# Optimization experiments

Measured on AMD Instinct MI355X. Metric: run time of the kernel, lower is better.

## Reference

```python
import jax, jax.numpy as jnp
import numpy as np


def setup_inputs() -> dict:
    key = jax.random.key(0)
    ks = jax.random.split(key, 5)
    B, T, C = 4, 2048, 2048
    n_heads = 16
    sc = 0.02
    return {
        "x": jax.random.normal(ks[0], (B, T, C), dtype=jnp.float32),
        "Wqkv": jax.random.normal(ks[1], (3 * C, C), dtype=jnp.float32) * sc,
        "bqkv": jax.random.normal(ks[2], (3 * C,), dtype=jnp.float32) * sc,
        "Wout": jax.random.normal(ks[3], (C, C), dtype=jnp.float32) * sc,
        "bout": jax.random.normal(ks[4], (C,), dtype=jnp.float32) * sc,
        "n_heads": n_heads,
    }


def reference(x, Wqkv, bqkv, Wout, bout, n_heads):
    B, T, C = x.shape
    hd = C // n_heads
    qkv = x @ Wqkv.T + bqkv                      # [B, T, 3C]
    q, k, v = jnp.split(qkv, 3, axis=-1)
    # [B, T, C] -> [B, nH, T, hd]
    def heads(t):
        return t.reshape(B, T, n_heads, hd).transpose(0, 2, 1, 3)
    q, k, v = heads(q), heads(k), heads(v)
    new_k, new_v = k, v
    att = jnp.einsum('bhqd,bhkd->bhqk', q, k) / jnp.sqrt(jnp.float32(hd))
    T_total = k.shape[2]
    # torch.tril(ones(T, T_total)): allow j <= i (standard causal when T_total == T)
    mask = jnp.tril(jnp.ones((T, T_total), dtype=bool))
    att = jnp.where(mask, att, -jnp.inf)
    att = jax.nn.softmax(att, axis=-1)
    y = jnp.einsum('bhqk,bhkd->bhqd', att, v)    # [B, nH, T, hd]
    y = y.transpose(0, 2, 1, 3).reshape(B, T, C)
    y = y @ Wout.T + bout
    return (y, new_k, new_v)
```

## Files before the change

kernel.cpp:

```cpp
#include <hip/hip_runtime.h>
#include <hip/hip_bf16.h>

typedef __attribute__((ext_vector_type(8))) short bf16x8;
typedef __attribute__((ext_vector_type(4))) float f32x4;

__device__ __forceinline__ unsigned short f2bf(float f) {
  unsigned u = __float_as_uint(f);
  u += 0x7fffu + ((u >> 16) & 1u);
  return (unsigned short)(u >> 16);
}

__device__ __forceinline__ void gload16(const void* g, void* l) {
  __builtin_amdgcn_global_load_lds(
      (const __attribute__((address_space(1))) void*)g,
      (__attribute__((address_space(3))) void*)l, 16, 0, 0);
}

__global__ void cvt_bf16(const float* __restrict__ in, unsigned short* __restrict__ out, int n4) {
  int i = blockIdx.x * blockDim.x + threadIdx.x;
  int st = gridDim.x * blockDim.x;
  for (; i < n4; i += st) {
    float4 f = ((const float4*)in)[i];
    ushort4 o;
    o.x = f2bf(f.x); o.y = f2bf(f.y); o.z = f2bf(f.z); o.w = f2bf(f.w);
    ((ushort4*)out)[i] = o;
  }
}

template<int EPI>
__global__ __launch_bounds__(512, 2) void gemm_bt(
    const unsigned short* __restrict__ A,
    const unsigned short* __restrict__ B,
    const float* __restrict__ bias,
    float* __restrict__ outF,
    unsigned short* __restrict__ q_ws,
    unsigned short* __restrict__ k_ws,
    unsigned short* __restrict__ v_wst,
    float* __restrict__ out_k,
    float* __restrict__ out_v,
    int M, int N, int K)
{
  __shared__ __align__(16) unsigned short As[2][16384];
  __shared__ __align__(16) unsigned short Bs[2][16384];

  const int nbx = N >> 8;
  int nwg = gridDim.x;
  int bid = blockIdx.x;
  int cpx = nwg >> 3;
  int sw  = (bid & 7) * cpx + (bid >> 3);
  int bx = sw % nbx, by = sw / nbx;
  const int m0 = by << 8, n0 = bx << 8;

  const int tid = threadIdx.x, w = tid >> 6, ln = tid & 63;
  const int wm = w >> 2, wn = w & 3;
  const int lg = ln >> 4, lc = ln & 15;

  const int srow = tid >> 3;
  const int scol = ((ln & 7) ^ (srow & 7)) * 8;

  f32x4 acc[8][4] = {};

  auto STAGE = [&](int bf, int k0) {
#pragma unroll
    for (int i = 0; i < 4; ++i)
      gload16(A + (size_t)(m0 + i * 64 + srow) * K + k0 + scol,
              &As[bf][i * 4096 + w * 512]);
#pragma unroll
    for (int i = 0; i < 4; ++i)
      gload16(B + (size_t)(n0 + i * 64 + srow) * K + k0 + scol,
              &Bs[bf][i * 4096 + w * 512]);
  };

  auto rdA = [&](const unsigned short* as, int mh, int mf, int ks) -> bf16x8 {
    int r = wm * 128 + mh * 64 + mf * 16 + lc;
    int cb = (ks * 64 + lg * 16) ^ ((r & 7) << 4);
    return *(const bf16x8*)((const char*)as + r * 128 + cb);
  };
  auto rdB = [&](const unsigned short* bs, int nh, int nf, int ks) -> bf16x8 {
    int r = wn * 64 + (nh * 2 + nf) * 16 + lc;
    int cb = (ks * 64 + lg * 16) ^ ((r & 7) << 4);
    return *(const bf16x8*)((const char*)bs + r * 128 + cb);
  };

  const int nt = K >> 6;
  STAGE(0, 0);
  for (int t = 0; t < nt; ++t) {
    const unsigned short* as = As[t & 1];
    const unsigned short* bs = Bs[t & 1];
    if (t + 1 < nt) {
      STAGE((t + 1) & 1, (t + 1) << 6);
      asm volatile("s_waitcnt vmcnt(8)" ::: "memory");
    } else {
      asm volatile("s_waitcnt vmcnt(0)" ::: "memory");
    }
    __builtin_amdgcn_sched_barrier(0);
    asm volatile("s_barrier" ::: "memory");
    __builtin_amdgcn_sched_barrier(0);

    bf16x8 a[4][2], b[2][2];
#pragma unroll
    for (int mf = 0; mf < 4; ++mf)
#pragma unroll
      for (int ks = 0; ks < 2; ++ks) a[mf][ks] = rdA(as, 0, mf, ks);
#pragma unroll
    for (int nf = 0; nf < 2; ++nf)
#pragma unroll
      for (int ks = 0; ks < 2; ++ks) b[nf][ks] = rdB(bs, 0, nf, ks);
    __builtin_amdgcn_s_setprio(1);
#pragma unroll
    for (int ks = 0; ks < 2; ++ks)
#pragma unroll
      for (int mf = 0; mf < 4; ++mf)
#pragma unroll
        for (int nf = 0; nf < 2; ++nf)
          acc[mf][nf] = __builtin_amdgcn_mfma_f32_16x16x32_bf16(a[mf][ks], b[nf][ks], acc[mf][nf], 0, 0, 0);
    __builtin_amdgcn_s_setprio(0);
#pragma unroll
    for (int nf = 0; nf < 2; ++nf)
#pragma unroll
      for (int ks = 0; ks < 2; ++ks) b[nf][ks] = rdB(bs, 1, nf, ks);
    __builtin_amdgcn_s_setprio(1);
#pragma unroll
    for (int ks = 0; ks < 2; ++ks)
#pragma unroll
      for (int mf = 0; mf < 4; ++mf)
#pragma unroll
        for (int nf = 0; nf < 2; ++nf)
          acc[mf][2 + nf] = __builtin_amdgcn_mfma_f32_16x16x32_bf16(a[mf][ks], b[nf][ks], acc[mf][2 + nf], 0, 0, 0);
    __builtin_amdgcn_s_setprio(0);
#pragma unroll
    for (int mf = 0; mf < 4; ++mf)
#pragma unroll
      for (int ks = 0; ks < 2; ++ks) a[mf][ks] = rdA(as, 1, mf, ks);
    __builtin_amdgcn_s_setprio(1);
#pragma unroll
    for (int ks = 0; ks < 2; ++ks)
#pragma unroll
      for (int mf = 0; mf < 4; ++mf)
#pragma unroll
        for (int nf = 0; nf < 2; ++nf)
          acc[4 + mf][2 + nf] = __builtin_amdgcn_mfma_f32_16x16x32_bf16(a[mf][ks], b[nf][ks], acc[4 + mf][2 + nf], 0, 0, 0);
    __builtin_amdgcn_s_setprio(0);
#pragma unroll
    for (int nf = 0; nf < 2; ++nf)
#pragma unroll
      for (int ks = 0; ks < 2; ++ks) b[nf][ks] = rdB(bs, 0, nf, ks);
    __builtin_amdgcn_s_setprio(1);
#pragma unroll
    for (int ks = 0; ks < 2; ++ks)
#pragma unroll
      for (int mf = 0; mf < 4; ++mf)
#pragma unroll
        for (int nf = 0; nf < 2; ++nf)
          acc[4 + mf][nf] = __builtin_amdgcn_mfma_f32_16x16x32_bf16(a[mf][ks], b[nf][ks], acc[4 + mf][nf], 0, 0, 0);
    __builtin_amdgcn_s_setprio(0);

    __builtin_amdgcn_sched_barrier(0);
    asm volatile("s_barrier" ::: "memory");
    __builtin_amdgcn_sched_barrier(0);
  }

  if (EPI == 0) {
#pragma unroll
    for (int m8 = 0; m8 < 8; ++m8) {
      int r0 = m0 + wm * 128 + m8 * 16 + lg * 4;
#pragma unroll
      for (int n4 = 0; n4 < 4; ++n4) {
        int c = n0 + wn * 64 + n4 * 16 + lc;
        float bv = bias[c];
#pragma unroll
        for (int r = 0; r < 4; ++r)
          outF[(size_t)(r0 + r) * N + c] = acc[m8][n4][r] + bv;
      }
    }
  } else {
    const int sel = n0 >> 11;
    const int b_  = m0 >> 11;
#pragma unroll
    for (int m8 = 0; m8 < 8; ++m8) {
      int t0 = (m0 & 2047) + wm * 128 + m8 * 16 + lg * 4;
#pragma unroll
      for (int n4 = 0; n4 < 4; ++n4) {
        int dg = n0 + wn * 64 + n4 * 16 + lc;
        int h  = (dg >> 7) & 15;
        int d  = dg & 127;
        const size_t hb = (size_t)(b_ * 16 + h);
        float bv = bias[dg];
        float v0 = acc[m8][n4][0] + bv, v1 = acc[m8][n4][1] + bv;
        float v2 = acc[m8][n4][2] + bv, v3 = acc[m8][n4][3] + bv;
        size_t base = (hb * 2048 + t0) * 128 + d;
        if (sel == 0) {
          q_ws[base      ] = f2bf(v0);
          q_ws[base + 128] = f2bf(v1);
          q_ws[base + 256] = f2bf(v2);
          q_ws[base + 384] = f2bf(v3);
        } else if (sel == 1) {
          out_k[base] = v0; out_k[base + 128] = v1; out_k[base + 256] = v2; out_k[base + 384] = v3;
          k_ws[base      ] = f2bf(v0);
          k_ws[base + 128] = f2bf(v1);
          k_ws[base + 256] = f2bf(v2);
          k_ws[base + 384] = f2bf(v3);
        } else {
          out_v[base] = v0; out_v[base + 128] = v1; out_v[base + 256] = v2; out_v[base + 384] = v3;
          ushort4 pk; pk.x = f2bf(v0); pk.y = f2bf(v1); pk.z = f2bf(v2); pk.w = f2bf(v3);
          *(ushort4*)&v_wst[(hb * 128 + d) * 2048 + t0] = pk;
        }
      }
    }
  }
}

__global__ __launch_bounds__(256) void attn_fwd(
    const unsigned short* __restrict__ q_ws,
    const unsigned short* __restrict__ k_ws,
    const unsigned short* __restrict__ v_wst,
    unsigned short* __restrict__ y_ws)
{
  __shared__ __align__(16) unsigned short K_lds[2][64 * 128];
  __shared__ __align__(16) unsigned short Vt_lds[2][128 * 64];
  __shared__ __align__(16) unsigned short P_lds[128 * 64];

  int bid = blockIdx.x;
  int sw = (bid & 7) * 128 + (bid >> 3);
  const int bh = sw >> 4;
  const int qb = sw & 15;
  const int q0 = qb << 7;
  const int tid = threadIdx.x, w = tid >> 6, ln = tid & 63;
  const int lg = ln >> 4, lc = ln & 15;
  const int b = bh >> 4, h = bh & 15;

  bf16x8 qf[2][4];
  {
    const unsigned short* qp = q_ws + ((size_t)bh * 2048 + q0 + w * 32) * 128;
#pragma unroll
    for (int m = 0; m < 2; ++m)
#pragma unroll
      for (int ks = 0; ks < 4; ++ks)
        qf[m][ks] = *(const bf16x8*)&qp[(m * 16 + lc) * 128 + ks * 32 + lg * 8];
  }

  float lsum[2] = {0.f, 0.f};
  f32x4 o[2][8] = {};

  auto STAGE = [&](int bf, int kv0) {
#pragma unroll
    for (int i = 0; i < 4; ++i) {
      int rowK = w * 16 + i * 4 + lg;
      int gK = (lc * 16) ^ ((rowK & 7) << 4);
      gload16(k_ws + ((size_t)bh * 2048 + kv0 + rowK) * 128 + (gK >> 1),
              &K_lds[bf][(w * 16 + i * 4) * 128]);
      int rowV = w * 32 + i * 8 + (ln >> 3);
      int gV = ((ln & 7) * 16) ^ ((rowV & 7) << 4);
      gload16(v_wst + ((size_t)bh * 128 + rowV) * 2048 + kv0 + (gV >> 1),
              &Vt_lds[bf][(w * 32 + i * 8) * 64]);
    }
  };

  const int ntiles = (q0 >> 6) + 2;
  STAGE(0, 0);
  const float scl = 0.08838834764831845f;

  for (int t = 0; t < ntiles; ++t) {
    const int kv0 = t << 6;
    __syncthreads();
    if (t + 1 < ntiles) STAGE((t + 1) & 1, (t + 1) << 6);
    if (kv0 > q0 + w * 32 + 31) continue;
    const unsigned short* Kl = K_lds[t & 1];
    const unsigned short* Vl = Vt_lds[t & 1];

    f32x4 s[2][4] = {};
#pragma unroll
    for (int ks = 0; ks < 4; ++ks) {
      bf16x8 kb[4];
#pragma unroll
      for (int n = 0; n < 4; ++n) {
        int row = n * 16 + lc;
        int cb = (ks * 64 + lg * 16) ^ ((row & 7) << 4);
        kb[n] = *(const bf16x8*)((const char*)Kl + row * 256 + cb);
      }
#pragma unroll
      for (int m = 0; m < 2; ++m)
#pragma unroll
        for (int n = 0; n < 4; ++n)
          s[m][n] = __builtin_amdgcn_mfma_f32_16x16x32_bf16(kb[n], qf[m][ks], s[m][n], 0, 0, 0);
    }

#pragma unroll
    for (int m = 0; m < 2; ++m) {
      const int rowg = q0 + w * 32 + m * 16 + lc;
      const int prow = w * 32 + m * 16 + lc;
      const unsigned swz = (unsigned)((prow & 7) << 4);
#pragma unroll
      for (int n = 0; n < 4; ++n) {
        const int colg = kv0 + n * 16 + lg * 4;
        float p0 = (colg + 0 > rowg) ? 0.f : __expf(s[m][n][0] * scl);
        float p1 = (colg + 1 > rowg) ? 0.f : __expf(s[m][n][1] * scl);
        float p2 = (colg + 2 > rowg) ? 0.f : __expf(s[m][n][2] * scl);
        float p3 = (colg + 3 > rowg) ? 0.f : __expf(s[m][n][3] * scl);
        lsum[m] += (p0 + p1) + (p2 + p3);
        ushort4 pk;
        pk.x = f2bf(p0); pk.y = f2bf(p1); pk.z = f2bf(p2); pk.w = f2bf(p3);
        *(ushort4*)((char*)P_lds + prow * 128 + ((unsigned)(n * 32 + lg * 8) ^ swz)) = pk;
      }
    }

#pragma unroll
    for (int ks = 0; ks < 2; ++ks) {
      bf16x8 pbf[2], vb[8];
#pragma unroll
      for (int m = 0; m < 2; ++m) {
        int prow = w * 32 + m * 16 + lc;
        int cb = (ks * 64 + lg * 16) ^ ((prow & 7) << 4);
        pbf[m] = *(const bf16x8*)((const char*)P_lds + prow * 128 + cb);
      }
#pragma unroll
      for (int n8 = 0; n8 < 8; ++n8) {
        int row = n8 * 16 + lc;
        int cb = (ks * 64 + lg * 16) ^ ((row & 7) << 4);
        vb[n8] = *(const bf16x8*)((const char*)Vl + row * 128 + cb);
      }
#pragma unroll
      for (int m = 0; m < 2; ++m)
#pragma unroll
        for (int n8 = 0; n8 < 8; ++n8)
          o[m][n8] = __builtin_amdgcn_mfma_f32_16x16x32_bf16(vb[n8], pbf[m], o[m][n8], 0, 0, 0);
    }
  }

  float inv[2];
#pragma unroll
  for (int m = 0; m < 2; ++m) {
    float ls = lsum[m];
    ls += __shfl_xor(ls, 16);
    ls += __shfl_xor(ls, 32);
    inv[m] = 1.f / ls;
  }
  const size_t bb = (size_t)b * 2048;
#pragma unroll
  for (int m = 0; m < 2; ++m) {
    int rowg = q0 + w * 32 + m * 16 + lc;
    unsigned short* yp = y_ws + (bb + rowg) * 2048 + h * 128;
#pragma unroll
    for (int n8 = 0; n8 < 8; ++n8) {
      ushort4 pk;
      pk.x = f2bf(o[m][n8][0] * inv[m]);
      pk.y = f2bf(o[m][n8][1] * inv[m]);
      pk.z = f2bf(o[m][n8][2] * inv[m]);
      pk.w = f2bf(o[m][n8][3] * inv[m]);
      *(ushort4*)&yp[n8 * 16 + lg * 4] = pk;
    }
  }
}

extern "C" void kernel_launch(void* const* d_in, const int* in_sizes, int n_in,
                              void* d_out, int out_size, void* d_ws, size_t ws_size,
                              hipStream_t stream) {
  const float* x    = (const float*)d_in[0];
  const float* Wqkv = (const float*)d_in[1];
  const float* bqkv = (const float*)d_in[2];
  const float* Wout = (const float*)d_in[3];
  const float* bout = (const float*)d_in[4];

  float* y_out = (float*)d_out;
  float* k_out = y_out + (size_t)16777216;
  float* v_out = y_out + (size_t)33554432;

  unsigned short* xb    = (unsigned short*)d_ws;
  unsigned short* wqkvb = xb + 16777216;
  unsigned short* woutb = wqkvb + 12582912;
  unsigned short* q_ws  = woutb + 4194304;
  unsigned short* k_ws  = q_ws + 16777216;
  unsigned short* v_wst = k_ws + 16777216;
  unsigned short* y_ws  = v_wst + 16777216;

  cvt_bf16<<<2048, 256, 0, stream>>>(x, xb, 16777216 / 4);
  cvt_bf16<<<2048, 256, 0, stream>>>(Wqkv, wqkvb, 12582912 / 4);
  cvt_bf16<<<1024, 256, 0, stream>>>(Wout, woutb, 4194304 / 4);

  gemm_bt<1><<<768, 512, 0, stream>>>(xb, wqkvb, bqkv, nullptr,
                                      q_ws, k_ws, v_wst, k_out, v_out,
                                      8192, 6144, 2048);

  attn_fwd<<<1024, 256, 0, stream>>>(q_ws, k_ws, v_wst, y_ws);

  gemm_bt<0><<<256, 512, 0, stream>>>(y_ws, woutb, bout, y_out,
                                      nullptr, nullptr, nullptr, nullptr, nullptr,
                                      8192, 2048, 2048);
}
```

Baseline: 740.1 us.

## Use 32x32 MFMA tiles in GEMM and single-buffer attention LDS for occupancy

The projection GEMM switches from 16x16x32 to 32x32x16 bf16 MFMA. Each wave now loads larger fragments with fewer LDS reads per unit of math, and the epilogue is remapped to the 32x32 accumulator layout. Extra workgroup barriers are added between the fragment loads and the MFMA phases. The attention kernel drops its K/V double buffer for a single buffer with synchronous staging and requests three blocks per SM via launch bounds. This trades prefetch overlap for higher occupancy, and adds a second sync per tile that exposes load latency.

Result: slower. 979.9 us (+32.4%).

```diff
diff --git a/kernel.cpp b/kernel.cpp
--- a/kernel.cpp
+++ b/kernel.cpp
@@ -3,6 +3,7 @@
 
 typedef __attribute__((ext_vector_type(8))) short bf16x8;
 typedef __attribute__((ext_vector_type(4))) float f32x4;
+typedef __attribute__((ext_vector_type(16))) float f32x16;
 
 __device__ __forceinline__ unsigned short f2bf(float f) {
   unsigned u = __float_as_uint(f);
@@ -53,12 +54,12 @@
 
   const int tid = threadIdx.x, w = tid >> 6, ln = tid & 63;
   const int wm = w >> 2, wn = w & 3;
-  const int lg = ln >> 4, lc = ln & 15;
+  const int l31 = ln & 31, lhi = ln >> 5;
 
   const int srow = tid >> 3;
   const int scol = ((ln & 7) ^ (srow & 7)) * 8;
 
-  f32x4 acc[8][4] = {};
+  f32x16 acc[4][2] = {};
 
   auto STAGE = [&](int bf, int k0) {
 #pragma unroll
@@ -71,14 +72,14 @@
               &Bs[bf][i * 4096 + w * 512]);
   };
 
-  auto rdA = [&](const unsigned short* as, int mh, int mf, int ks) -> bf16x8 {
-    int r = wm * 128 + mh * 64 + mf * 16 + lc;
-    int cb = (ks * 64 + lg * 16) ^ ((r & 7) << 4);
+  auto rdA = [&](const unsigned short* as, int mb, int ks) -> bf16x8 {
+    int r = wm * 128 + mb * 32 + l31;
+    int cb = ((ks * 2 + lhi) << 4) ^ ((r & 7) << 4);
     return *(const bf16x8*)((const char*)as + r * 128 + cb);
   };
-  auto rdB = [&](const unsigned short* bs, int nh, int nf, int ks) -> bf16x8 {
-    int r = wn * 64 + (nh * 2 + nf) * 16 + lc;
-    int cb = (ks * 64 + lg * 16) ^ ((r & 7) << 4);
+  auto rdB = [&](const unsigned short* bs, int nb, int ks) -> bf16x8 {
+    int r = wn * 64 + nb * 32 + l31;
+    int cb = ((ks * 2 + lhi) << 4) ^ ((r & 7) << 4);
     return *(const bf16x8*)((const char*)bs + r * 128 + cb);
   };
 
@@ -97,63 +98,43 @@
     asm volatile("s_barrier" ::: "memory");
     __builtin_amdgcn_sched_barrier(0);
 
-    bf16x8 a[4][2], b[2][2];
-#pragma unroll
-    for (int mf = 0; mf < 4; ++mf)
-#pragma unroll
-      for (int ks = 0; ks < 2; ++ks) a[mf][ks] = rdA(as, 0, mf, ks);
-#pragma unroll
-    for (int nf = 0; nf < 2; ++nf)
-#pragma unroll
-      for (int ks = 0; ks < 2; ++ks) b[nf][ks] = rdB(bs, 0, nf, ks);
+    bf16x8 a[2][4], b[2][4];
+#pragma unroll
+    for (int mb = 0; mb < 2; ++mb)
+#pragma unroll
+      for (int ks = 0; ks < 4; ++ks) a[mb][ks] = rdA(as, mb, ks);
+#pragma unroll
+    for (int nb = 0; nb < 2; ++nb)
+#pragma unroll
+      for (int ks = 0; ks < 4; ++ks) b[nb][ks] = rdB(bs, nb, ks);
+    __builtin_amdgcn_sched_barrier(0);
+    asm volatile("s_barrier" ::: "memory");
+    __builtin_amdgcn_sched_barrier(0);
     __builtin_amdgcn_s_setprio(1);
 #pragma unroll
-    for (int ks = 0; ks < 2; ++ks)
-#pragma unroll
-      for (int mf = 0; mf < 4; ++mf)
-#pragma unroll
-        for (int nf = 0; nf < 2; ++nf)
-          acc[mf][nf] = __builtin_amdgcn_mfma_f32_16x16x32_bf16(a[mf][ks], b[nf][ks], acc[mf][nf], 0, 0, 0);
+    for (int ks = 0; ks < 4; ++ks)
+#pragma unroll
+      for (int mb = 0; mb < 2; ++mb)
+#pragma unroll
+        for (int nb = 0; nb < 2; ++nb)
+          acc[mb][nb] = __builtin_amdgcn_mfma_f32_32x32x16_bf16(a[mb][ks], b[nb][ks], acc[mb][nb], 0, 0, 0);
     __builtin_amdgcn_s_setprio(0);
 #pragma unroll
-    for (int nf = 0; nf < 2; ++nf)
-#pragma unroll
-      for (int ks = 0; ks < 2; ++ks) b[nf][ks] = rdB(bs, 1, nf, ks);
+    for (int mb = 0; mb < 2; ++mb)
+#pragma unroll
+      for (int ks = 0; ks < 4; ++ks) a[mb][ks] = rdA(as, 2 + mb, ks);
+    __builtin_amdgcn_sched_barrier(0);
+    asm volatile("s_barrier" ::: "memory");
+    __builtin_amdgcn_sched_barrier(0);
     __builtin_amdgcn_s_setprio(1);
 #pragma unroll
-    for (int ks = 0; ks < 2; ++ks)
-#pragma unroll
-      for (int mf = 0; mf < 4; ++mf)
-#pragma unroll
-        for (int nf = 0; nf < 2; ++nf)
-          acc[mf][2 + nf] = __builtin_amdgcn_mfma_f32_16x16x32_bf16(a[mf][ks], b[nf][ks], acc[mf][2 + nf], 0, 0, 0);
+    for (int ks = 0; ks < 4; ++ks)
+#pragma unroll
+      for (int mb = 0; mb < 2; ++mb)
+#pragma unroll
+        for (int nb = 0; nb < 2; ++nb)
+          acc[2 + mb][nb] = __builtin_amdgcn_mfma_f32_32x32x16_bf16(a[mb][ks], b[nb][ks], acc[2 + mb][nb], 0, 0, 0);
     __builtin_amdgcn_s_setprio(0);
-#pragma unroll
-    for (int mf = 0; mf < 4; ++mf)
-#pragma unroll
-      for (int ks = 0; ks < 2; ++ks) a[mf][ks] = rdA(as, 1, mf, ks);
-    __builtin_amdgcn_s_setprio(1);
-#pragma unroll
-    for (int ks = 0; ks < 2; ++ks)
-#pragma unroll
-      for (int mf = 0; mf < 4; ++mf)
-#pragma unroll
-        for (int nf = 0; nf < 2; ++nf)
-          acc[4 + mf][2 + nf] = __builtin_amdgcn_mfma_f32_16x16x32_bf16(a[mf][ks], b[nf][ks], acc[4 + mf][2 + nf], 0, 0, 0);
-    __builtin_amdgcn_s_setprio(0);
-#pragma unroll
-    for (int nf = 0; nf < 2; ++nf)
-#pragma unroll
-      for (int ks = 0; ks < 2; ++ks) b[nf][ks] = rdB(bs, 0, nf, ks);
-    __builtin_amdgcn_s_setprio(1);
-#pragma unroll
-    for (int ks = 0; ks < 2; ++ks)
-#pragma unroll
-      for (int mf = 0; mf < 4; ++mf)
-#pragma unroll
-        for (int nf = 0; nf < 2; ++nf)
-          acc[4 + mf][nf] = __builtin_amdgcn_mfma_f32_16x16x32_bf16(a[mf][ks], b[nf][ks], acc[4 + mf][nf], 0, 0, 0);
-    __builtin_amdgcn_s_setprio(0);
 
     __builtin_amdgcn_sched_barrier(0);
     asm volatile("s_barrier" ::: "memory");
@@ -162,62 +143,70 @@
 
   if (EPI == 0) {
 #pragma unroll
-    for (int m8 = 0; m8 < 8; ++m8) {
-      int r0 = m0 + wm * 128 + m8 * 16 + lg * 4;
-#pragma unroll
-      for (int n4 = 0; n4 < 4; ++n4) {
-        int c = n0 + wn * 64 + n4 * 16 + lc;
+    for (int mb = 0; mb < 4; ++mb) {
+#pragma unroll
+      for (int nb = 0; nb < 2; ++nb) {
+        int c = n0 + wn * 64 + nb * 32 + l31;
         float bv = bias[c];
 #pragma unroll
-        for (int r = 0; r < 4; ++r)
-          outF[(size_t)(r0 + r) * N + c] = acc[m8][n4][r] + bv;
+        for (int g = 0; g < 4; ++g) {
+          int r0 = m0 + wm * 128 + mb * 32 + g * 8 + lhi * 4;
+#pragma unroll
+          for (int i = 0; i < 4; ++i)
+            outF[(size_t)(r0 + i) * N + c] = acc[mb][nb][g * 4 + i] + bv;
+        }
       }
     }
   } else {
     const int sel = n0 >> 11;
     const int b_  = m0 >> 11;
 #pragma unroll
-    for (int m8 = 0; m8 < 8; ++m8) {
-      int t0 = (m0 & 2047) + wm * 128 + m8 * 16 + lg * 4;
-#pragma unroll
-      for (int n4 = 0; n4 < 4; ++n4) {
-        int dg = n0 + wn * 64 + n4 * 16 + lc;
+    for (int mb = 0; mb < 4; ++mb) {
+#pragma unroll
+      for (int nb = 0; nb < 2; ++nb) {
+        int dg = n0 + wn * 64 + nb * 32 + l31;
         int h  = (dg >> 7) & 15;
         int d  = dg & 127;
         const size_t hb = (size_t)(b_ * 16 + h);
         float bv = bias[dg];
-        float v0 = acc[m8][n4][0] + bv, v1 = acc[m8][n4][1] + bv;
-        float v2 = acc[m8][n4][2] + bv, v3 = acc[m8][n4][3] + bv;
-        size_t base = (hb * 2048 + t0) * 128 + d;
-        if (sel == 0) {
-          q_ws[base      ] = f2bf(v0);
-          q_ws[base + 128] = f2bf(v1);
-          q_ws[base + 256] = f2bf(v2);
-          q_ws[base + 384] = f2bf(v3);
-        } else if (sel == 1) {
-          out_k[base] = v0; out_k[base + 128] = v1; out_k[base + 256] = v2; out_k[base + 384] = v3;
-          k_ws[base      ] = f2bf(v0);
-          k_ws[base + 128] = f2bf(v1);
-          k_ws[base + 256] = f2bf(v2);
-          k_ws[base + 384] = f2bf(v3);
-        } else {
-          out_v[base] = v0; out_v[base + 128] = v1; out_v[base + 256] = v2; out_v[base + 384] = v3;
-          ushort4 pk; pk.x = f2bf(v0); pk.y = f2bf(v1); pk.z = f2bf(v2); pk.w = f2bf(v3);
-          *(ushort4*)&v_wst[(hb * 128 + d) * 2048 + t0] = pk;
+#pragma unroll
+        for (int g = 0; g < 4; ++g) {
+          int t0 = (m0 & 2047) + wm * 128 + mb * 32 + g * 8 + lhi * 4;
+          size_t base = (hb * 2048 + t0) * 128 + d;
+          float v0 = acc[mb][nb][g * 4 + 0] + bv;
+          float v1 = acc[mb][nb][g * 4 + 1] + bv;
+          float v2 = acc[mb][nb][g * 4 + 2] + bv;
+          float v3 = acc[mb][nb][g * 4 + 3] + bv;
+          if (sel == 0) {
+            q_ws[base      ] = f2bf(v0);
+            q_ws[base + 128] = f2bf(v1);
+            q_ws[base + 256] = f2bf(v2);
+            q_ws[base + 384] = f2bf(v3);
+          } else if (sel == 1) {
+            out_k[base] = v0; out_k[base + 128] = v1; out_k[base + 256] = v2; out_k[base + 384] = v3;
+            k_ws[base      ] = f2bf(v0);
+            k_ws[base + 128] = f2bf(v1);
+            k_ws[base + 256] = f2bf(v2);
+            k_ws[base + 384] = f2bf(v3);
+          } else {
+            out_v[base] = v0; out_v[base + 128] = v1; out_v[base + 256] = v2; out_v[base + 384] = v3;
+            ushort4 pk; pk.x = f2bf(v0); pk.y = f2bf(v1); pk.z = f2bf(v2); pk.w = f2bf(v3);
+            *(ushort4*)&v_wst[(hb * 128 + d) * 2048 + t0] = pk;
+          }
         }
       }
     }
   }
 }
 
-__global__ __launch_bounds__(256) void attn_fwd(
+__global__ __launch_bounds__(256, 3) void attn_fwd(
     const unsigned short* __restrict__ q_ws,
     const unsigned short* __restrict__ k_ws,
     const unsigned short* __restrict__ v_wst,
     unsigned short* __restrict__ y_ws)
 {
-  __shared__ __align__(16) unsigned short K_lds[2][64 * 128];
-  __shared__ __align__(16) unsigned short Vt_lds[2][128 * 64];
+  __shared__ __align__(16) unsigned short K_lds[64 * 128];
+  __shared__ __align__(16) unsigned short Vt_lds[128 * 64];
   __shared__ __align__(16) unsigned short P_lds[128 * 64];
 
   int bid = blockIdx.x;
@@ -242,31 +231,29 @@
   float lsum[2] = {0.f, 0.f};
   f32x4 o[2][8] = {};
 
-  auto STAGE = [&](int bf, int kv0) {
+  auto STAGE = [&](int kv0) {
 #pragma unroll
     for (int i = 0; i < 4; ++i) {
       int rowK = w * 16 + i * 4 + lg;
       int gK = (lc * 16) ^ ((rowK & 7) << 4);
       gload16(k_ws + ((size_t)bh * 2048 + kv0 + rowK) * 128 + (gK >> 1),
-              &K_lds[bf][(w * 16 + i * 4) * 128]);
+              &K_lds[(w * 16 + i * 4) * 128]);
       int rowV = w * 32 + i * 8 + (ln >> 3);
       int gV = ((ln & 7) * 16) ^ ((rowV & 7) << 4);
       gload16(v_wst + ((size_t)bh * 128 + rowV) * 2048 + kv0 + (gV >> 1),
-              &Vt_lds[bf][(w * 32 + i * 8) * 64]);
+              &Vt_lds[(w * 32 + i * 8) * 64]);
     }
   };
 
   const int ntiles = (q0 >> 6) + 2;
-  STAGE(0, 0);
   const float scl = 0.08838834764831845f;
 
   for (int t = 0; t < ntiles; ++t) {
     const int kv0 = t << 6;
     __syncthreads();
-    if (t + 1 < ntiles) STAGE((t + 1) & 1, (t + 1) << 6);
+    STAGE(kv0);
+    __syncthreads();
     if (kv0 > q0 + w * 32 + 31) continue;
-    const unsigned short* Kl = K_lds[t & 1];
-    const unsigned short* Vl = Vt_lds[t & 1];
 
     f32x4 s[2][4] = {};
 #pragma unroll
@@ -276,7 +263,7 @@
       for (int n = 0; n < 4; ++n) {
         int row = n * 16 + lc;
         int cb = (ks * 64 + lg * 16) ^ ((row & 7) << 4);
-        kb[n] = *(const bf16x8*)((const char*)Kl + row * 256 + cb);
+        kb[n] = *(const bf16x8*)((const char*)K_lds + row * 256 + cb);
       }
 #pragma unroll
       for (int m = 0; m < 2; ++m)
@@ -317,7 +304,7 @@
       for (int n8 = 0; n8 < 8; ++n8) {
         int row = n8 * 16 + lc;
         int cb = (ks * 64 + lg * 16) ^ ((row & 7) << 4);
-        vb[n8] = *(const bf16x8*)((const char*)Vl + row * 128 + cb);
+        vb[n8] = *(const bf16x8*)((const char*)Vt_lds + row * 128 + cb);
       }
 #pragma unroll
       for (int m = 0; m < 2; ++m)
```
